# Optimization experiments

Hardware: AMD Instinct MI355X
Metric: run time of the kernel (lower is better)

The kernel has to match this reference:

```python
import jax, jax.numpy as jnp
import numpy as np

N_NODES = 100000
N_EDGES = 1600000
N_GRAPHS = 64
IN_FEATS = 86  # 10 + |NodeTypes|(3) + |Devices|(5) + 2*2 + 2*32
GCN_H = 64
FC_H = 32
BN_EPS = 1e-5


def setup_inputs() -> dict:
    key = jax.random.key(0)
    ks = jax.random.split(key, 10)
    x = jax.random.normal(ks[0], (N_NODES, IN_FEATS), dtype=jnp.float32)
    edge_src = jax.random.randint(ks[1], (N_EDGES,), 0, N_NODES, dtype=jnp.int32)
    edge_dst = jax.random.randint(ks[2], (N_EDGES,), 0, N_NODES, dtype=jnp.int32)
    graph_ids = jnp.sort(jax.random.randint(ks[3], (N_NODES,), 0, N_GRAPHS, dtype=jnp.int32))
    bn_gamma = jnp.ones((IN_FEATS,), dtype=jnp.float32)
    bn_beta = jnp.zeros((IN_FEATS,), dtype=jnp.float32)
    W1 = jax.random.normal(ks[4], (IN_FEATS, GCN_H), dtype=jnp.float32) * 0.1
    b1 = jnp.zeros((GCN_H,), dtype=jnp.float32)
    W2 = jax.random.normal(ks[5], (GCN_H, GCN_H), dtype=jnp.float32) * 0.1
    b2 = jnp.zeros((GCN_H,), dtype=jnp.float32)
    fc1_w = jax.random.normal(ks[6], (GCN_H, FC_H), dtype=jnp.float32) * 0.1
    fc1_b = jnp.zeros((FC_H,), dtype=jnp.float32)
    fc2_w = jax.random.normal(ks[7], (FC_H, 1), dtype=jnp.float32) * 0.1
    fc2_b = jnp.zeros((1,), dtype=jnp.float32)
    return {"x": x, "edge_src": edge_src, "edge_dst": edge_dst,
            "graph_ids": graph_ids, "num_graphs": N_GRAPHS,
            "bn_gamma": bn_gamma, "bn_beta": bn_beta,
            "W1": W1, "b1": b1, "W2": W2, "b2": b2,
            "fc1_w": fc1_w, "fc1_b": fc1_b, "fc2_w": fc2_w, "fc2_b": fc2_b}


def _gcn_layer(h, edge_src, edge_dst, W, b):
    # DGL copy_src + mean reduce: each node's h is overwritten by the mean of
    # its in-neighbors' h; zero-in-degree nodes keep their old h (UDF reduce
    # is only applied to nodes with non-empty mailboxes).
    n = h.shape[0]
    msg_sum = jax.ops.segment_sum(h[edge_src], edge_dst, num_segments=n)  # [N, d]
    deg = jax.ops.segment_sum(jnp.ones_like(edge_dst, dtype=h.dtype), edge_dst, num_segments=n)
    agg = jnp.where(deg[:, None] > 0, msg_sum / jnp.maximum(deg, 1.0)[:, None], h)
    return jax.nn.relu(agg @ W + b)


def reference(x, edge_src, edge_dst, graph_ids, num_graphs,
              bn_gamma, bn_beta, W1, b1, W2, b2, fc1_w, fc1_b, fc2_w, fc2_b):
    # BatchNorm1d in training mode: batch stats, biased variance.
    mean = jnp.mean(x, axis=0)
    var = jnp.mean(jnp.square(x - mean), axis=0)
    h = (x - mean) * jax.lax.rsqrt(var + BN_EPS) * bn_gamma + bn_beta
    # Two GCN layers (mean message passing + linear + ReLU).
    h = _gcn_layer(h, edge_src, edge_dst, W1, b1)
    h = _gcn_layer(h, edge_src, edge_dst, W2, b2)
    # dgl.mean_nodes over the batched graph: per-graph mean of node features.
    g_sum = jax.ops.segment_sum(h, graph_ids, num_segments=num_graphs)  # [B, d]
    g_cnt = jax.ops.segment_sum(jnp.ones_like(graph_ids, dtype=h.dtype), graph_ids, num_segments=num_graphs)
    hg = g_sum / jnp.maximum(g_cnt, 1.0)[:, None]
    # FC head (no activation between the two linears, matching the source).
    hg = hg @ fc1_w + fc1_b
    hg = hg @ fc2_w + fc2_b
    return jax.nn.sigmoid(hg).squeeze()
```

## Files before the change

### kernel.cpp

```cpp
#include <hip/hip_runtime.h>

#define N_NODES 100000
#define N_EDGES 1600000
#define N_GRAPHS_C 64
#define IN_F 86
#define H 64
#define N_BKT 391
#define SC_EPT 8
#define SC_TILE 2048
#define SC_GRID 782
#define BC_GRID 1024
#define NW_POOL 2048
typedef unsigned short ushort;

__device__ inline float bf2f(ushort u) { return __uint_as_float(((unsigned)u) << 16); }
__device__ inline ushort f2bf(float f) {
    unsigned x = __float_as_uint(f);
    return (ushort)((x + 0x7fffu + ((x >> 16) & 1u)) >> 16);
}

__global__ void bn_count_k(const float* __restrict__ x, const int* __restrict__ dst,
                           float* __restrict__ bnsum, float* __restrict__ bnsq,
                           int* __restrict__ bcnt) {
    __shared__ float s1[IN_F], s2[IN_F];
    __shared__ int hist[N_BKT];
    int tid = threadIdx.x;
    if (tid < IN_F) { s1[tid] = 0.f; s2[tid] = 0.f; }
    for (int i = tid; i < N_BKT; i += 256) hist[i] = 0;
    __syncthreads();
    if (blockIdx.x < SC_GRID) {
        int e0 = blockIdx.x * SC_TILE;
#pragma unroll
        for (int i = 0; i < SC_EPT; i++) {
            int e = e0 + i * 256 + tid;
            if (e < N_EDGES) atomicAdd(&hist[dst[e] >> 8], 1);
        }
    }
    const int NWAVE = BC_GRID * 4;
    const int RPW = (N_NODES + NWAVE - 1) / NWAVE;
    int lane = tid & 63;
    int w = blockIdx.x * 4 + (tid >> 6);
    int r0 = w * RPW;
    int r1 = min(r0 + RPW, N_NODES);
    float sum0 = 0.f, sq0 = 0.f, sum1 = 0.f, sq1 = 0.f;
#pragma unroll 4
    for (int r = r0; r < r1; r++) {
        const float* base = x + (size_t)r * IN_F;
        float v0 = base[lane];
        float v1 = (lane < IN_F - 64) ? base[64 + lane] : 0.f;
        sum0 += v0; sq0 += v0 * v0;
        sum1 += v1; sq1 += v1 * v1;
    }
    atomicAdd(&s1[lane], sum0);
    atomicAdd(&s2[lane], sq0);
    if (lane < IN_F - 64) {
        atomicAdd(&s1[64 + lane], sum1);
        atomicAdd(&s2[64 + lane], sq1);
    }
    __syncthreads();
    if (tid < IN_F) {
        atomicAdd(&bnsum[tid], s1[tid]);
        atomicAdd(&bnsq[tid], s2[tid]);
    }
    if (blockIdx.x < SC_GRID)
        for (int i = tid; i < N_BKT; i += 256) atomicAdd(&bcnt[i], hist[i]);
}

__global__ void scanprep_k(const int* __restrict__ bcnt, int* __restrict__ bstart,
                           int* __restrict__ gcursor,
                           const float* __restrict__ bnsum, const float* __restrict__ bnsq,
                           const float* __restrict__ gamma, const float* __restrict__ beta,
                           const float* __restrict__ W1, const float* __restrict__ b1,
                           float* __restrict__ W1p, float* __restrict__ c1) {
    __shared__ int tmp[512];
    __shared__ float scale[IN_F], shift[IN_F];
    int t = threadIdx.x;
    int v = (t < N_BKT) ? bcnt[t] : 0;
    tmp[t] = v;
    __syncthreads();
    for (int off = 1; off < 512; off <<= 1) {
        int a = (t >= off) ? tmp[t - off] : 0;
        __syncthreads();
        tmp[t] += a;
        __syncthreads();
    }
    if (t < N_BKT) { bstart[t] = tmp[t] - v; gcursor[t] = tmp[t] - v; }
    if (t == N_BKT - 1) bstart[N_BKT] = tmp[t];
    if (t < IN_F) {
        float mean = bnsum[t] * (1.0f / N_NODES);
        float var  = bnsq[t] * (1.0f / N_NODES) - mean * mean;
        float sc = gamma[t] * rsqrtf(var + 1e-5f);
        scale[t] = sc;
        shift[t] = beta[t] - mean * sc;
    }
    __syncthreads();
    for (int idx = t; idx < IN_F * H; idx += 512) W1p[idx] = scale[idx / H] * W1[idx];
    if (t < H) {
        float acc = b1[t];
        for (int i = 0; i < IN_F; i++) acc += shift[i] * W1[i * H + t];
        c1[t] = acc;
    }
}

__global__ void bucket_scatter_k(const int* __restrict__ src, const int* __restrict__ dst,
                                 int* __restrict__ gcursor, unsigned* __restrict__ ebkt) {
    __shared__ int hist[N_BKT];
    __shared__ int base[N_BKT];
    int tid = threadIdx.x;
    for (int i = tid; i < N_BKT; i += 256) hist[i] = 0;
    __syncthreads();
    int e0 = blockIdx.x * SC_TILE;
    unsigned pk[SC_EPT];
    int bk[SC_EPT], lo[SC_EPT];
#pragma unroll
    for (int i = 0; i < SC_EPT; i++) {
        int e = e0 + i * 256 + tid;
        if (e < N_EDGES) {
            int d = dst[e];
            pk[i] = ((unsigned)src[e] << 8) | (unsigned)(d & 255);
            bk[i] = d >> 8;
            lo[i] = atomicAdd(&hist[bk[i]], 1);
        }
    }
    __syncthreads();
    for (int i = tid; i < N_BKT; i += 256) base[i] = atomicAdd(&gcursor[i], hist[i]);
    __syncthreads();
#pragma unroll
    for (int i = 0; i < SC_EPT; i++) {
        int e = e0 + i * 256 + tid;
        if (e < N_EDGES) ebkt[base[bk[i]] + lo[i]] = pk[i];
    }
}

__global__ void bucket_fill_k(const unsigned* __restrict__ ebkt, const int* __restrict__ bstart,
                              int* __restrict__ rs, int* __restrict__ csr) {
    __shared__ int deg[256];
    __shared__ int scn[256];
    __shared__ int cur[256];
    int b = blockIdx.x;
    int tid = threadIdx.x;
    int e0 = bstart[b], e1 = bstart[b + 1];
    deg[tid] = 0;
    __syncthreads();
    for (int e = e0 + tid; e < e1; e += 256) atomicAdd(&deg[ebkt[e] & 255u], 1);
    __syncthreads();
    scn[tid] = deg[tid];
    __syncthreads();
    for (int off = 1; off < 256; off <<= 1) {
        int a = (tid >= off) ? scn[tid - off] : 0;
        __syncthreads();
        scn[tid] += a;
        __syncthreads();
    }
    int node = (b << 8) + tid;
    if (node < N_NODES) rs[node] = e0 + scn[tid];
    cur[tid] = e0 + scn[tid] - deg[tid];
    __syncthreads();
    for (int e = e0 + tid; e < e1; e += 256) {
        unsigned p = ebkt[e];
        int pos = atomicAdd(&cur[p & 255u], 1);
        csr[pos] = (int)((p & ~255u) >> 1);
    }
}

__global__ __launch_bounds__(256) void gemm_f32_k(const float* __restrict__ X,
                                                  const float* __restrict__ W,
                                                  const float* __restrict__ bias,
                                                  ushort* __restrict__ Y, int N) {
    const int K = IN_F;
    __shared__ __align__(16) float Xl[64][IN_F + 1];
    __shared__ __align__(16) float Wl[IN_F][64];
    int tid = threadIdx.x;
    int row0 = blockIdx.x * 64;
    for (int i = tid; i < K * 64; i += 256) Wl[i / 64][i % 64] = W[i];
    for (int i = tid; i < 64 * K; i += 256) {
        int r = i / K, c = i % K;
        Xl[r][c] = (row0 + r < N) ? X[(size_t)(row0 + r) * K + c] : 0.f;
    }
    __syncthreads();
    int cg = tid & 15, rg = tid >> 4;
    float4 b4 = *(const float4*)&bias[cg * 4];
    float acc[4][4];
    for (int i = 0; i < 4; i++) { acc[i][0] = b4.x; acc[i][1] = b4.y; acc[i][2] = b4.z; acc[i][3] = b4.w; }
    for (int k = 0; k < K; k++) {
        float4 w = *(const float4*)&Wl[k][cg * 4];
        float x0 = Xl[rg * 4 + 0][k];
        float x1 = Xl[rg * 4 + 1][k];
        float x2 = Xl[rg * 4 + 2][k];
        float x3 = Xl[rg * 4 + 3][k];
        acc[0][0] += x0 * w.x; acc[0][1] += x0 * w.y; acc[0][2] += x0 * w.z; acc[0][3] += x0 * w.w;
        acc[1][0] += x1 * w.x; acc[1][1] += x1 * w.y; acc[1][2] += x1 * w.z; acc[1][3] += x1 * w.w;
        acc[2][0] += x2 * w.x; acc[2][1] += x2 * w.y; acc[2][2] += x2 * w.z; acc[2][3] += x2 * w.w;
        acc[3][0] += x3 * w.x; acc[3][1] += x3 * w.y; acc[3][2] += x3 * w.z; acc[3][3] += x3 * w.w;
    }
    for (int i = 0; i < 4; i++) {
        int gr = row0 + rg * 4 + i;
        if (gr < N) {
            ushort4 o;
            o.x = f2bf(acc[i][0]); o.y = f2bf(acc[i][1]);
            o.z = f2bf(acc[i][2]); o.w = f2bf(acc[i][3]);
            *(ushort4*)&Y[(size_t)gr * 64 + cg * 4] = o;
        }
    }
}

__global__ __launch_bounds__(256) void gemm_bf16_k(const ushort* __restrict__ X,
                                                   const float* __restrict__ W,
                                                   const float* __restrict__ bias,
                                                   ushort* __restrict__ Y, int N) {
    const int K = H;
    __shared__ __align__(16) float Xl[64][H + 1];
    __shared__ __align__(16) float Wl[H][64];
    int tid = threadIdx.x;
    int row0 = blockIdx.x * 64;
    for (int i = tid; i < K * 64; i += 256) Wl[i / 64][i % 64] = W[i];
    for (int i = tid; i < 64 * 16; i += 256) {
        int r = i >> 4, c4 = (i & 15) * 4;
        if (row0 + r < N) {
            ushort4 u = *(const ushort4*)&X[(size_t)(row0 + r) * K + c4];
            Xl[r][c4 + 0] = bf2f(u.x); Xl[r][c4 + 1] = bf2f(u.y);
            Xl[r][c4 + 2] = bf2f(u.z); Xl[r][c4 + 3] = bf2f(u.w);
        } else {
            Xl[r][c4 + 0] = 0.f; Xl[r][c4 + 1] = 0.f;
            Xl[r][c4 + 2] = 0.f; Xl[r][c4 + 3] = 0.f;
        }
    }
    __syncthreads();
    int cg = tid & 15, rg = tid >> 4;
    float4 b4 = *(const float4*)&bias[cg * 4];
    float acc[4][4];
    for (int i = 0; i < 4; i++) { acc[i][0] = b4.x; acc[i][1] = b4.y; acc[i][2] = b4.z; acc[i][3] = b4.w; }
    for (int k = 0; k < K; k++) {
        float4 w = *(const float4*)&Wl[k][cg * 4];
        float x0 = Xl[rg * 4 + 0][k];
        float x1 = Xl[rg * 4 + 1][k];
        float x2 = Xl[rg * 4 + 2][k];
        float x3 = Xl[rg * 4 + 3][k];
        acc[0][0] += x0 * w.x; acc[0][1] += x0 * w.y; acc[0][2] += x0 * w.z; acc[0][3] += x0 * w.w;
        acc[1][0] += x1 * w.x; acc[1][1] += x1 * w.y; acc[1][2] += x1 * w.z; acc[1][3] += x1 * w.w;
        acc[2][0] += x2 * w.x; acc[2][1] += x2 * w.y; acc[2][2] += x2 * w.z; acc[2][3] += x2 * w.w;
        acc[3][0] += x3 * w.x; acc[3][1] += x3 * w.y; acc[3][2] += x3 * w.z; acc[3][3] += x3 * w.w;
    }
    for (int i = 0; i < 4; i++) {
        int gr = row0 + rg * 4 + i;
        if (gr < N) {
            ushort4 o;
            o.x = f2bf(acc[i][0]); o.y = f2bf(acc[i][1]);
            o.z = f2bf(acc[i][2]); o.w = f2bf(acc[i][3]);
            *(ushort4*)&Y[(size_t)gr * 64 + cg * 4] = o;
        }
    }
}

__device__ inline void gather_row2(const char* __restrict__ gB, const int* __restrict__ csr,
                                   int start, int end, int lane, float& olo, float& ohi) {
    int half = lane >> 5;
    int fl = lane & 31;
    const char* gL = gB + (fl << 2);
    float lo0 = 0.f, lo1 = 0.f, lo2 = 0.f, lo3 = 0.f;
    float lo4 = 0.f, lo5 = 0.f, lo6 = 0.f, lo7 = 0.f;
    float hi0 = 0.f, hi1 = 0.f, hi2 = 0.f, hi3 = 0.f;
    float hi4 = 0.f, hi5 = 0.f, hi6 = 0.f, hi7 = 0.f;
    for (int j0 = start; j0 < end; j0 += 64) {
        int cnt = min(64, end - j0);
        int myoff = (lane < cnt) ? csr[j0 + lane] : 0;
        int j = 0;
        for (; j + 16 <= cnt; j += 16) {
            int s0 = __shfl(myoff, j + 0 + half, 64);
            int s1 = __shfl(myoff, j + 2 + half, 64);
            int s2 = __shfl(myoff, j + 4 + half, 64);
            int s3 = __shfl(myoff, j + 6 + half, 64);
            int s4 = __shfl(myoff, j + 8 + half, 64);
            int s5 = __shfl(myoff, j + 10 + half, 64);
            int s6 = __shfl(myoff, j + 12 + half, 64);
            int s7 = __shfl(myoff, j + 14 + half, 64);
            unsigned u0 = *(const unsigned*)(gL + s0);
            unsigned u1 = *(const unsigned*)(gL + s1);
            unsigned u2 = *(const unsigned*)(gL + s2);
            unsigned u3 = *(const unsigned*)(gL + s3);
            unsigned u4 = *(const unsigned*)(gL + s4);
            unsigned u5 = *(const unsigned*)(gL + s5);
            unsigned u6 = *(const unsigned*)(gL + s6);
            unsigned u7 = *(const unsigned*)(gL + s7);
            lo0 += __uint_as_float(u0 << 16); hi0 += __uint_as_float(u0 & 0xffff0000u);
            lo1 += __uint_as_float(u1 << 16); hi1 += __uint_as_float(u1 & 0xffff0000u);
            lo2 += __uint_as_float(u2 << 16); hi2 += __uint_as_float(u2 & 0xffff0000u);
            lo3 += __uint_as_float(u3 << 16); hi3 += __uint_as_float(u3 & 0xffff0000u);
            lo4 += __uint_as_float(u4 << 16); hi4 += __uint_as_float(u4 & 0xffff0000u);
            lo5 += __uint_as_float(u5 << 16); hi5 += __uint_as_float(u5 & 0xffff0000u);
            lo6 += __uint_as_float(u6 << 16); hi6 += __uint_as_float(u6 & 0xffff0000u);
            lo7 += __uint_as_float(u7 << 16); hi7 += __uint_as_float(u7 & 0xffff0000u);
        }
        for (; j < cnt; j += 2) {
            int idx = j + half;
            int s = __shfl(myoff, (idx < cnt) ? idx : (cnt - 1), 64);
            unsigned u = *(const unsigned*)(gL + s);
            if (idx < cnt) {
                lo0 += __uint_as_float(u << 16);
                hi0 += __uint_as_float(u & 0xffff0000u);
            }
        }
    }
    float lo = ((lo0 + lo1) + (lo2 + lo3)) + ((lo4 + lo5) + (lo6 + lo7));
    float hi = ((hi0 + hi1) + (hi2 + hi3)) + ((hi4 + hi5) + (hi6 + hi7));
    lo += __shfl_xor(lo, 32, 64);
    hi += __shfl_xor(hi, 32, 64);
    olo = lo; ohi = hi;
}

__global__ void gather_k(const ushort* __restrict__ g, const int* __restrict__ rs,
                         const int* __restrict__ csr, ushort* __restrict__ out) {
    int lane = threadIdx.x & 63;
    int n = blockIdx.x * 4 + (threadIdx.x >> 6);
    if (n >= N_NODES) return;
    int start = (n == 0) ? 0 : rs[n - 1];
    int end = rs[n];
    float lo, hi;
    gather_row2((const char*)g, csr, start, end, lane, lo, hi);
    int d = end - start;
    int fl = lane & 31;
    float vlo, vhi;
    if (d > 0) {
        float inv = 1.0f / (float)d;
        vlo = lo * inv; vhi = hi * inv;
    } else {
        unsigned u = *(const unsigned*)((const char*)g + (size_t)n * 128 + (fl << 2));
        vlo = __uint_as_float(u << 16);
        vhi = __uint_as_float(u & 0xffff0000u);
    }
    vlo = fmaxf(vlo, 0.f); vhi = fmaxf(vhi, 0.f);
    if (lane < 32) {
        ushort2 o; o.x = f2bf(vlo); o.y = f2bf(vhi);
        *(ushort2*)((char*)out + (size_t)n * 128 + (fl << 2)) = o;
    }
}

__global__ void pool_k(const ushort* __restrict__ h, const int* __restrict__ gid,
                       float* __restrict__ gsum, int* __restrict__ gcnt) {
    int lane = threadIdx.x & 63;
    int wpb = blockDim.x >> 6;
    int gw = blockIdx.x * wpb + (threadIdx.x >> 6);
    const int chunk = (N_NODES + NW_POOL - 1) / NW_POOL;
    int n0 = gw * chunk;
    if (n0 >= N_NODES) return;
    int n1 = min(n0 + chunk, N_NODES);
    float acc = 0.f;
    int cur = gid[n0], cnt = 0;
    for (int n = n0; n < n1; n++) {
        int g = gid[n];
        if (g != cur) {
            atomicAdd(&gsum[cur * H + lane], acc);
            if (lane == 0) atomicAdd(&gcnt[cur], cnt);
            cur = g; acc = 0.f; cnt = 0;
        }
        acc += bf2f(h[(size_t)n * H + lane]);
        cnt++;
    }
    atomicAdd(&gsum[cur * H + lane], acc);
    if (lane == 0) atomicAdd(&gcnt[cur], cnt);
}

__global__ void head_k(const float* __restrict__ gsum, const int* __restrict__ gcnt,
                       const float* __restrict__ fc1w, const float* __restrict__ fc1b,
                       const float* __restrict__ fc2w, const float* __restrict__ fc2b,
                       float* __restrict__ out) {
    __shared__ float w1[H * 32];
    __shared__ float w2[32], bb1[32];
    int b = threadIdx.x;
    for (int i = b; i < H * 32; i += 64) w1[i] = fc1w[i];
    if (b < 32) { w2[b] = fc2w[b]; bb1[b] = fc1b[b]; }
    __syncthreads();
    if (b >= N_GRAPHS_C) return;
    float hg[H];
    float inv = 1.0f / fmaxf((float)gcnt[b], 1.0f);
    for (int k = 0; k < H; k++) hg[k] = gsum[b * H + k] * inv;
    float z = fc2b[0];
    for (int j = 0; j < 32; j++) {
        float t = bb1[j];
        for (int k = 0; k < H; k++) t += hg[k] * w1[k * 32 + j];
        z += t * w2[j];
    }
    out[b] = 1.0f / (1.0f + expf(-z));
}

extern "C" void kernel_launch(void* const* d_in, const int* in_sizes, int n_in,
                              void* d_out, int out_size, void* d_ws, size_t ws_size,
                              hipStream_t stream) {
    const float* x        = (const float*)d_in[0];
    const int*   edge_src = (const int*)d_in[1];
    const int*   edge_dst = (const int*)d_in[2];
    const int*   gid      = (const int*)d_in[3];
    const float* bn_gamma = (const float*)d_in[5];
    const float* bn_beta  = (const float*)d_in[6];
    const float* W1       = (const float*)d_in[7];
    const float* b1       = (const float*)d_in[8];
    const float* W2       = (const float*)d_in[9];
    const float* b2       = (const float*)d_in[10];
    const float* fc1w     = (const float*)d_in[11];
    const float* fc1b     = (const float*)d_in[12];
    const float* fc2w     = (const float*)d_in[13];
    const float* fc2b     = (const float*)d_in[14];
    float* out = (float*)d_out;

    char* ws = (char*)d_ws;
    size_t off = 0;
    auto alloc = [&](size_t bytes) { void* p = ws + off; off += (bytes + 255) & ~(size_t)255; return p; };
    const size_t ZW = IN_F + IN_F + N_BKT + N_GRAPHS_C * H + N_GRAPHS_C;
    float* zreg  = (float*)alloc(ZW * sizeof(float));
    float* bnsum = zreg;
    float* bnsq  = bnsum + IN_F;
    int*   bcnt  = (int*)(bnsq + IN_F);
    float* gsum  = (float*)(bcnt + N_BKT);
    int*   gcnt  = (int*)(gsum + N_GRAPHS_C * H);
    float* W1p     = (float*)alloc(IN_F * H * sizeof(float));
    float* c1      = (float*)alloc(H * sizeof(float));
    int*   bstart  = (int*)alloc((N_BKT + 1) * sizeof(int));
    int*   gcursor = (int*)alloc(N_BKT * sizeof(int));
    int*   rs      = (int*)alloc(N_NODES * sizeof(int));
    int*   csr     = (int*)alloc((size_t)N_EDGES * sizeof(int));
    ushort* gbuf   = (ushort*)alloc((size_t)N_NODES * H * sizeof(ushort));
    ushort* h1     = (ushort*)alloc((size_t)N_NODES * H * sizeof(ushort));
    unsigned* ebkt = (unsigned*)gbuf;

    hipMemsetAsync(zreg, 0, ZW * sizeof(float), stream);

    bn_count_k<<<BC_GRID, 256, 0, stream>>>(x, edge_dst, bnsum, bnsq, bcnt);
    scanprep_k<<<1, 512, 0, stream>>>(bcnt, bstart, gcursor, bnsum, bnsq,
                                      bn_gamma, bn_beta, W1, b1, W1p, c1);
    bucket_scatter_k<<<SC_GRID, 256, 0, stream>>>(edge_src, edge_dst, gcursor, ebkt);
    bucket_fill_k<<<N_BKT, 256, 0, stream>>>(ebkt, bstart, rs, csr);

    gemm_f32_k<<<(N_NODES + 63) / 64, 256, 0, stream>>>(x, W1p, c1, gbuf, N_NODES);
    gather_k<<<(N_NODES + 3) / 4, 256, 0, stream>>>(gbuf, rs, csr, h1);

    gemm_bf16_k<<<(N_NODES + 63) / 64, 256, 0, stream>>>(h1, W2, b2, gbuf, N_NODES);
    gather_k<<<(N_NODES + 3) / 4, 256, 0, stream>>>(gbuf, rs, csr, h1);

    pool_k<<<NW_POOL / 4, 256, 0, stream>>>(h1, gid, gsum, gcnt);
    head_k<<<1, 64, 0, stream>>>(gsum, gcnt, fc1w, fc1b, fc2w, fc2b, out);
}
```

Before: 398.8 us.

## Transpose GEMM X tile in LDS and widen gather to 8-byte loads

Both GEMM kernels now store the input tile transposed in shared memory, padded to 68 columns, so each thread reads its four row values with one float4 LDS load instead of four scalar loads. The gather kernel is restructured so 16 lanes cover a 128-byte row with 8-byte loads, and four edge groups run in parallel per wave. Partial sums are then combined with two cross-lane xor shuffles. This aims to cut load instruction count in both kernels, but the gather keeps fewer independent loads in flight per lane, with two accumulators instead of eight, which may reduce latency hiding.

```diff
diff --git a/kernel.cpp b/kernel.cpp
--- a/kernel.cpp
+++ b/kernel.cpp
@@ -168,14 +168,14 @@
                                                   const float* __restrict__ bias,
                                                   ushort* __restrict__ Y, int N) {
     const int K = IN_F;
-    __shared__ __align__(16) float Xl[64][IN_F + 1];
+    __shared__ __align__(16) float Xt[IN_F][68];
     __shared__ __align__(16) float Wl[IN_F][64];
     int tid = threadIdx.x;
     int row0 = blockIdx.x * 64;
     for (int i = tid; i < K * 64; i += 256) Wl[i / 64][i % 64] = W[i];
     for (int i = tid; i < 64 * K; i += 256) {
         int r = i / K, c = i % K;
-        Xl[r][c] = (row0 + r < N) ? X[(size_t)(row0 + r) * K + c] : 0.f;
+        Xt[c][r] = (row0 + r < N) ? X[(size_t)(row0 + r) * K + c] : 0.f;
     }
     __syncthreads();
     int cg = tid & 15, rg = tid >> 4;
@@ -184,14 +184,11 @@
     for (int i = 0; i < 4; i++) { acc[i][0] = b4.x; acc[i][1] = b4.y; acc[i][2] = b4.z; acc[i][3] = b4.w; }
     for (int k = 0; k < K; k++) {
         float4 w = *(const float4*)&Wl[k][cg * 4];
-        float x0 = Xl[rg * 4 + 0][k];
-        float x1 = Xl[rg * 4 + 1][k];
-        float x2 = Xl[rg * 4 + 2][k];
-        float x3 = Xl[rg * 4 + 3][k];
-        acc[0][0] += x0 * w.x; acc[0][1] += x0 * w.y; acc[0][2] += x0 * w.z; acc[0][3] += x0 * w.w;
-        acc[1][0] += x1 * w.x; acc[1][1] += x1 * w.y; acc[1][2] += x1 * w.z; acc[1][3] += x1 * w.w;
-        acc[2][0] += x2 * w.x; acc[2][1] += x2 * w.y; acc[2][2] += x2 * w.z; acc[2][3] += x2 * w.w;
-        acc[3][0] += x3 * w.x; acc[3][1] += x3 * w.y; acc[3][2] += x3 * w.z; acc[3][3] += x3 * w.w;
+        float4 xv = *(const float4*)&Xt[k][rg * 4];
+        acc[0][0] += xv.x * w.x; acc[0][1] += xv.x * w.y; acc[0][2] += xv.x * w.z; acc[0][3] += xv.x * w.w;
+        acc[1][0] += xv.y * w.x; acc[1][1] += xv.y * w.y; acc[1][2] += xv.y * w.z; acc[1][3] += xv.y * w.w;
+        acc[2][0] += xv.z * w.x; acc[2][1] += xv.z * w.y; acc[2][2] += xv.z * w.z; acc[2][3] += xv.z * w.w;
+        acc[3][0] += xv.w * w.x; acc[3][1] += xv.w * w.y; acc[3][2] += xv.w * w.z; acc[3][3] += xv.w * w.w;
     }
     for (int i = 0; i < 4; i++) {
         int gr = row0 + rg * 4 + i;
@@ -209,7 +206,7 @@
                                                    const float* __restrict__ bias,
                                                    ushort* __restrict__ Y, int N) {
     const int K = H;
-    __shared__ __align__(16) float Xl[64][H + 1];
+    __shared__ __align__(16) float Xt[H][68];
     __shared__ __align__(16) float Wl[H][64];
     int tid = threadIdx.x;
     int row0 = blockIdx.x * 64;
@@ -218,11 +215,11 @@
         int r = i >> 4, c4 = (i & 15) * 4;
         if (row0 + r < N) {
             ushort4 u = *(const ushort4*)&X[(size_t)(row0 + r) * K + c4];
-            Xl[r][c4 + 0] = bf2f(u.x); Xl[r][c4 + 1] = bf2f(u.y);
-            Xl[r][c4 + 2] = bf2f(u.z); Xl[r][c4 + 3] = bf2f(u.w);
+            Xt[c4 + 0][r] = bf2f(u.x); Xt[c4 + 1][r] = bf2f(u.y);
+            Xt[c4 + 2][r] = bf2f(u.z); Xt[c4 + 3][r] = bf2f(u.w);
         } else {
-            Xl[r][c4 + 0] = 0.f; Xl[r][c4 + 1] = 0.f;
-            Xl[r][c4 + 2] = 0.f; Xl[r][c4 + 3] = 0.f;
+            Xt[c4 + 0][r] = 0.f; Xt[c4 + 1][r] = 0.f;
+            Xt[c4 + 2][r] = 0.f; Xt[c4 + 3][r] = 0.f;
         }
     }
     __syncthreads();
@@ -232,14 +229,11 @@
     for (int i = 0; i < 4; i++) { acc[i][0] = b4.x; acc[i][1] = b4.y; acc[i][2] = b4.z; acc[i][3] = b4.w; }
     for (int k = 0; k < K; k++) {
         float4 w = *(const float4*)&Wl[k][cg * 4];
-        float x0 = Xl[rg * 4 + 0][k];
-        float x1 = Xl[rg * 4 + 1][k];
-        float x2 = Xl[rg * 4 + 2][k];
-        float x3 = Xl[rg * 4 + 3][k];
-        acc[0][0] += x0 * w.x; acc[0][1] += x0 * w.y; acc[0][2] += x0 * w.z; acc[0][3] += x0 * w.w;
-        acc[1][0] += x1 * w.x; acc[1][1] += x1 * w.y; acc[1][2] += x1 * w.z; acc[1][3] += x1 * w.w;
-        acc[2][0] += x2 * w.x; acc[2][1] += x2 * w.y; acc[2][2] += x2 * w.z; acc[2][3] += x2 * w.w;
-        acc[3][0] += x3 * w.x; acc[3][1] += x3 * w.y; acc[3][2] += x3 * w.z; acc[3][3] += x3 * w.w;
+        float4 xv = *(const float4*)&Xt[k][rg * 4];
+        acc[0][0] += xv.x * w.x; acc[0][1] += xv.x * w.y; acc[0][2] += xv.x * w.z; acc[0][3] += xv.x * w.w;
+        acc[1][0] += xv.y * w.x; acc[1][1] += xv.y * w.y; acc[1][2] += xv.y * w.z; acc[1][3] += xv.y * w.w;
+        acc[2][0] += xv.z * w.x; acc[2][1] += xv.z * w.y; acc[2][2] += xv.z * w.z; acc[2][3] += xv.z * w.w;
+        acc[3][0] += xv.w * w.x; acc[3][1] += xv.w * w.y; acc[3][2] += xv.w * w.z; acc[3][3] += xv.w * w.w;
     }
     for (int i = 0; i < 4; i++) {
         int gr = row0 + rg * 4 + i;
@@ -252,62 +246,6 @@
     }
 }
 
-__device__ inline void gather_row2(const char* __restrict__ gB, const int* __restrict__ csr,
-                                   int start, int end, int lane, float& olo, float& ohi) {
-    int half = lane >> 5;
-    int fl = lane & 31;
-    const char* gL = gB + (fl << 2);
-    float lo0 = 0.f, lo1 = 0.f, lo2 = 0.f, lo3 = 0.f;
-    float lo4 = 0.f, lo5 = 0.f, lo6 = 0.f, lo7 = 0.f;
-    float hi0 = 0.f, hi1 = 0.f, hi2 = 0.f, hi3 = 0.f;
-    float hi4 = 0.f, hi5 = 0.f, hi6 = 0.f, hi7 = 0.f;
-    for (int j0 = start; j0 < end; j0 += 64) {
-        int cnt = min(64, end - j0);
-        int myoff = (lane < cnt) ? csr[j0 + lane] : 0;
-        int j = 0;
-        for (; j + 16 <= cnt; j += 16) {
-            int s0 = __shfl(myoff, j + 0 + half, 64);
-            int s1 = __shfl(myoff, j + 2 + half, 64);
-            int s2 = __shfl(myoff, j + 4 + half, 64);
-            int s3 = __shfl(myoff, j + 6 + half, 64);
-            int s4 = __shfl(myoff, j + 8 + half, 64);
-            int s5 = __shfl(myoff, j + 10 + half, 64);
-            int s6 = __shfl(myoff, j + 12 + half, 64);
-            int s7 = __shfl(myoff, j + 14 + half, 64);
-            unsigned u0 = *(const unsigned*)(gL + s0);
-            unsigned u1 = *(const unsigned*)(gL + s1);
-            unsigned u2 = *(const unsigned*)(gL + s2);
-            unsigned u3 = *(const unsigned*)(gL + s3);
-            unsigned u4 = *(const unsigned*)(gL + s4);
-            unsigned u5 = *(const unsigned*)(gL + s5);
-            unsigned u6 = *(const unsigned*)(gL + s6);
-            unsigned u7 = *(const unsigned*)(gL + s7);
-            lo0 += __uint_as_float(u0 << 16); hi0 += __uint_as_float(u0 & 0xffff0000u);
-            lo1 += __uint_as_float(u1 << 16); hi1 += __uint_as_float(u1 & 0xffff0000u);
-            lo2 += __uint_as_float(u2 << 16); hi2 += __uint_as_float(u2 & 0xffff0000u);
-            lo3 += __uint_as_float(u3 << 16); hi3 += __uint_as_float(u3 & 0xffff0000u);
-            lo4 += __uint_as_float(u4 << 16); hi4 += __uint_as_float(u4 & 0xffff0000u);
-            lo5 += __uint_as_float(u5 << 16); hi5 += __uint_as_float(u5 & 0xffff0000u);
-            lo6 += __uint_as_float(u6 << 16); hi6 += __uint_as_float(u6 & 0xffff0000u);
-            lo7 += __uint_as_float(u7 << 16); hi7 += __uint_as_float(u7 & 0xffff0000u);
-        }
-        for (; j < cnt; j += 2) {
-            int idx = j + half;
-            int s = __shfl(myoff, (idx < cnt) ? idx : (cnt - 1), 64);
-            unsigned u = *(const unsigned*)(gL + s);
-            if (idx < cnt) {
-                lo0 += __uint_as_float(u << 16);
-                hi0 += __uint_as_float(u & 0xffff0000u);
-            }
-        }
-    }
-    float lo = ((lo0 + lo1) + (lo2 + lo3)) + ((lo4 + lo5) + (lo6 + lo7));
-    float hi = ((hi0 + hi1) + (hi2 + hi3)) + ((hi4 + hi5) + (hi6 + hi7));
-    lo += __shfl_xor(lo, 32, 64);
-    hi += __shfl_xor(hi, 32, 64);
-    olo = lo; ohi = hi;
-}
-
 __global__ void gather_k(const ushort* __restrict__ g, const int* __restrict__ rs,
                          const int* __restrict__ csr, ushort* __restrict__ out) {
     int lane = threadIdx.x & 63;
@@ -315,23 +253,63 @@
     if (n >= N_NODES) return;
     int start = (n == 0) ? 0 : rs[n - 1];
     int end = rs[n];
-    float lo, hi;
-    gather_row2((const char*)g, csr, start, end, lane, lo, hi);
-    int d = end - start;
-    int fl = lane & 31;
-    float vlo, vhi;
-    if (d > 0) {
-        float inv = 1.0f / (float)d;
-        vlo = lo * inv; vhi = hi * inv;
-    } else {
-        unsigned u = *(const unsigned*)((const char*)g + (size_t)n * 128 + (fl << 2));
-        vlo = __uint_as_float(u << 16);
-        vhi = __uint_as_float(u & 0xffff0000u);
-    }
-    vlo = fmaxf(vlo, 0.f); vhi = fmaxf(vhi, 0.f);
-    if (lane < 32) {
-        ushort2 o; o.x = f2bf(vlo); o.y = f2bf(vhi);
-        *(ushort2*)((char*)out + (size_t)n * 128 + (fl << 2)) = o;
+    int fl = lane & 15;
+    int grp = lane >> 4;
+    const char* gL = (const char*)g + (fl << 3);
+    float a0 = 0.f, a1 = 0.f, a2 = 0.f, a3 = 0.f;
+    float b0 = 0.f, b1 = 0.f, b2 = 0.f, b3 = 0.f;
+    for (int j0 = start; j0 < end; j0 += 64) {
+        int cnt = min(64, end - j0);
+        int myoff = (lane < cnt) ? csr[j0 + lane] : 0;
+        int j = 0;
+        for (; j + 8 <= cnt; j += 8) {
+            int s0 = __shfl(myoff, j + grp, 64);
+            int s1 = __shfl(myoff, j + 4 + grp, 64);
+            uint2 u0 = *(const uint2*)(gL + s0);
+            uint2 u1 = *(const uint2*)(gL + s1);
+            a0 += __uint_as_float(u0.x << 16);
+            a1 += __uint_as_float(u0.x & 0xffff0000u);
+            a2 += __uint_as_float(u0.y << 16);
+            a3 += __uint_as_float(u0.y & 0xffff0000u);
+            b0 += __uint_as_float(u1.x << 16);
+            b1 += __uint_as_float(u1.x & 0xffff0000u);
+            b2 += __uint_as_float(u1.y << 16);
+            b3 += __uint_as_float(u1.y & 0xffff0000u);
+        }
+        for (; j < cnt; j += 4) {
+            int idx = j + grp;
+            int s = __shfl(myoff, (idx < cnt) ? idx : (cnt - 1), 64);
+            uint2 u = *(const uint2*)(gL + s);
+            if (idx < cnt) {
+                a0 += __uint_as_float(u.x << 16);
+                a1 += __uint_as_float(u.x & 0xffff0000u);
+                a2 += __uint_as_float(u.y << 16);
+                a3 += __uint_as_float(u.y & 0xffff0000u);
+            }
+        }
+    }
+    float v0 = a0 + b0, v1 = a1 + b1, v2 = a2 + b2, v3 = a3 + b3;
+    v0 += __shfl_xor(v0, 16, 64); v0 += __shfl_xor(v0, 32, 64);
+    v1 += __shfl_xor(v1, 16, 64); v1 += __shfl_xor(v1, 32, 64);
+    v2 += __shfl_xor(v2, 16, 64); v2 += __shfl_xor(v2, 32, 64);
+    v3 += __shfl_xor(v3, 16, 64); v3 += __shfl_xor(v3, 32, 64);
+    if (grp == 0) {
+        int d = end - start;
+        float r0, r1, r2, r3;
+        if (d > 0) {
+            float inv = 1.0f / (float)d;
+            r0 = v0 * inv; r1 = v1 * inv; r2 = v2 * inv; r3 = v3 * inv;
+        } else {
+            uint2 u = *(const uint2*)((const char*)g + (size_t)n * 128 + (fl << 3));
+            r0 = __uint_as_float(u.x << 16);
+            r1 = __uint_as_float(u.x & 0xffff0000u);
+            r2 = __uint_as_float(u.y << 16);
+            r3 = __uint_as_float(u.y & 0xffff0000u);
+        }
+        ushort4 o;
+        o.x = f2bf(fmaxf(r0, 0.f)); o.y = f2bf(fmaxf(r1, 0.f));
+        o.z = f2bf(fmaxf(r2, 0.f)); o.w = f2bf(fmaxf(r3, 0.f));
+        *(ushort4*)((char*)out + (size_t)n * 128 + (fl << 3)) = o;
     }
 }
 
```

New measurement: 384.4 us. -3.6%, faster.
